# Kernel optimization log

Measured on AMD Instinct MI355X. Metric: run time of the kernel, lower is better.

## Reference

```python
import jax, jax.numpy as jnp
import numpy as np

B, T, C, NH = 8, 1024, 768, 12
HD = C // NH


def setup_inputs() -> dict:
    key = jax.random.key(0)
    k1, k2, k3, k4, k5 = jax.random.split(key, 5)
    s = 0.02
    return {
        "x": jax.random.normal(k1, (B, T, C), dtype=jnp.float32),
        "w_attn": jax.random.normal(k2, (C, 3 * C), dtype=jnp.float32) * s,
        "b_attn": jax.random.normal(k3, (3 * C,), dtype=jnp.float32) * s,
        "w_proj": jax.random.normal(k4, (C, C), dtype=jnp.float32) * s,
        "b_proj": jax.random.normal(k5, (C,), dtype=jnp.float32) * s,
    }


def reference(x, w_attn, b_attn, w_proj, b_proj):
    Bv, Tv, Cv = x.shape
    # fused QKV projection
    qkv = jnp.einsum('btc,cd->btd', x, w_attn) + b_attn  # [B,T,3C]
    q, k, v = jnp.split(qkv, 3, axis=-1)
    # [B, NH, T, HD]
    q = q.reshape(Bv, Tv, NH, HD).transpose(0, 2, 1, 3)
    k = k.reshape(Bv, Tv, NH, HD).transpose(0, 2, 1, 3)
    v = v.reshape(Bv, Tv, NH, HD).transpose(0, 2, 1, 3)
    scale = 1.0 / np.sqrt(HD).astype(np.float32)
    att = jnp.einsum('bhqd,bhkd->bhqk', q, k) * scale  # [B,NH,T,T]
    causal = jnp.tril(jnp.ones((Tv, Tv), dtype=bool))
    att = jnp.where(causal, att, -jnp.inf)
    att = jax.nn.softmax(att, axis=-1)
    y = jnp.einsum('bhqk,bhkd->bhqd', att, v)  # [B,NH,T,HD]
    y = y.transpose(0, 2, 1, 3).reshape(Bv, Tv, Cv)
    return jnp.einsum('btc,cd->btd', y, w_proj) + b_proj
```

## Files before the change

kernel.cpp:

```cpp
#include <hip/hip_runtime.h>

constexpr int kB  = 8;
constexpr int kT  = 1024;
constexpr int kC  = 768;
constexpr int kNH = 12;
constexpr int kHD = 64;
constexpr int kM  = kB * kT;
constexpr int k3C = 3 * kC;
constexpr int kQK = 2 * kC;

using bf16x8 = __attribute__((ext_vector_type(8))) __bf16;
using f32x4  = __attribute__((ext_vector_type(4))) float;

__device__ __forceinline__ unsigned short f2bf(float f) {
    union { float f; unsigned int u; } v; v.f = f;
    unsigned int r = v.u + 0x7fffu + ((v.u >> 16) & 1u);
    return (unsigned short)(r >> 16);
}

__device__ __forceinline__ void async16(const void* g, void* l) {
    __builtin_amdgcn_global_load_lds(
        (__attribute__((address_space(1))) void*)g,
        (__attribute__((address_space(3))) void*)l, 16, 0, 0);
}

template<int IMM> __device__ __forceinline__ void wait_vm() {
    __builtin_amdgcn_s_waitcnt(IMM);
}
__device__ __forceinline__ void wait_vm0() { __builtin_amdgcn_s_waitcnt(0x0F70); }


__global__ __launch_bounds__(256) void cvt_bf16_kernel(
    const float* __restrict__ in, unsigned short* __restrict__ out)
{
    const int i = blockIdx.x * 256 + threadIdx.x;
    const float4 v = ((const float4*)in)[i];
    ushort4 o;
    o.x = f2bf(v.x); o.y = f2bf(v.y); o.z = f2bf(v.z); o.w = f2bf(v.w);
    ((ushort4*)out)[i] = o;
}

__global__ __launch_bounds__(256) void transpose_cvt_kernel(
    const float* __restrict__ W, unsigned short* __restrict__ Wt, int K, int N)
{
    __shared__ float tile[32][33];
    const int tx = threadIdx.x & 31, ty = threadIdx.x >> 5;
    const int n0 = blockIdx.x * 32, k0 = blockIdx.y * 32;
    #pragma unroll
    for (int i = 0; i < 4; ++i)
        tile[ty + i * 8][tx] = W[(size_t)(k0 + ty + i * 8) * N + n0 + tx];
    __syncthreads();
    #pragma unroll
    for (int i = 0; i < 4; ++i)
        Wt[(size_t)(n0 + ty + i * 8) * K + k0 + tx] = f2bf(tile[tx][ty + i * 8]);
}

template<int NSUB, int MODE>
__global__ __launch_bounds__(256) void gemm_mfma_kernel(
    const unsigned short* __restrict__ A, int lda,
    const unsigned short* __restrict__ Bt,
    const float* __restrict__ bias,
    void* __restrict__ outv,
    unsigned short* __restrict__ vt,
    int N, int K)
{
    constexpr int NW = NSUB / 2;
    constexpr int BB = (NSUB / 4 > 0) ? NSUB / 4 : 1;
    constexpr int P  = 2 + BB;
    constexpr int WAIT_P = 0x0F70 | P;

    alignas(16) __shared__ unsigned short As[3][8 * 512];
    alignas(16) __shared__ unsigned short Bs[3][NSUB * 512];

    const int tid  = threadIdx.x;
    const int w    = tid >> 6;
    const int lane = tid & 63;
    const int wr = w >> 1, wc = w & 1;
    const int m0 = blockIdx.y * 128, n0 = blockIdx.x * (NSUB * 16);

    const int fr = lane & 15;
    const int fk = (lane >> 4) * 8;

    auto stage = [&](int bufi, int kt) {
        #pragma unroll
        for (int t = 0; t < 2; ++t) {
            const int fa = w * 2 + t;
            const unsigned short* ga =
                A + (size_t)(m0 + fa * 16 + fr) * lda + kt + fk;
            async16(ga, &As[bufi][fa * 512]);
        }
        #pragma unroll
        for (int t = 0; t < BB; ++t) {
            const int fb = w * BB + t;
            const unsigned short* gb =
                Bt + (size_t)(n0 + fb * 16 + fr) * K + kt + fk;
            async16(gb, &Bs[bufi][fb * 512]);
        }
    };

    f32x4 acc[4][NW];
    #pragma unroll
    for (int i = 0; i < 4; ++i)
        #pragma unroll
        for (int j = 0; j < NW; ++j) {
            f32x4 z = {0.f, 0.f, 0.f, 0.f};
            acc[i][j] = z;
        }

    const int niter = K / 32;
    stage(0, 0);
    stage(1, 32);
    int cur = 0, pf = 2;
    for (int it = 0; it < niter; ++it) {
        if (it + 1 < niter) wait_vm<WAIT_P>();
        else               wait_vm<0x0F70>();
        __builtin_amdgcn_s_barrier();
        if (it + 2 < niter) stage(pf, (it + 2) * 32);

        bf16x8 a[4], b[NW];
        #pragma unroll
        for (int i = 0; i < 4; ++i)
            a[i] = *(const bf16x8*)&As[cur][(wr * 4 + i) * 512 + lane * 8];
        #pragma unroll
        for (int j = 0; j < NW; ++j)
            b[j] = *(const bf16x8*)&Bs[cur][(wc * NW + j) * 512 + lane * 8];
        #pragma unroll
        for (int i = 0; i < 4; ++i)
            #pragma unroll
            for (int j = 0; j < NW; ++j)
                acc[i][j] = __builtin_amdgcn_mfma_f32_16x16x32_bf16(
                    a[i], b[j], acc[i][j], 0, 0, 0);

        cur = (cur == 2) ? 0 : cur + 1;
        pf  = (pf  == 2) ? 0 : pf  + 1;
    }

    const int quad  = lane >> 4;
    const int col16 = lane & 15;
    float biasv[NW];
    #pragma unroll
    for (int j = 0; j < NW; ++j)
        biasv[j] = bias[n0 + wc * (NW * 16) + j * 16 + col16];

    if (MODE == 1 && n0 >= kQK) {
        const int bidx = m0 >> 10;
        #pragma unroll
        for (int i = 0; i < 4; ++i) {
            const int row = m0 + wr * 64 + i * 16 + quad * 4;
            const int t = row & 1023;
            #pragma unroll
            for (int j = 0; j < NW; ++j) {
                const int hv = n0 + wc * (NW * 16) + j * 16 + col16 - kQK;
                const int h = hv >> 6, d = hv & 63;
                ushort4 o;
                o.x = f2bf(acc[i][j][0] + biasv[j]);
                o.y = f2bf(acc[i][j][1] + biasv[j]);
                o.z = f2bf(acc[i][j][2] + biasv[j]);
                o.w = f2bf(acc[i][j][3] + biasv[j]);
                *(ushort4*)&vt[((size_t)(bidx * kNH + h) * kHD + d) * kT + t] = o;
            }
        }
    } else {
        #pragma unroll
        for (int i = 0; i < 4; ++i) {
            #pragma unroll
            for (int r = 0; r < 4; ++r) {
                const int row = m0 + wr * 64 + i * 16 + quad * 4 + r;
                #pragma unroll
                for (int j = 0; j < NW; ++j) {
                    const int col = n0 + wc * (NW * 16) + j * 16 + col16;
                    const float v = acc[i][j][r] + biasv[j];
                    if (MODE == 1)
                        ((unsigned short*)outv)[(size_t)row * kQK + col] = f2bf(v);
                    else
                        ((float*)outv)[(size_t)row * N + col] = v;
                }
            }
        }
    }
}

__global__ __launch_bounds__(256) void attn_mfma_kernel(
    const unsigned short* __restrict__ qkv2,
    const unsigned short* __restrict__ VT,
    unsigned short* __restrict__ y)
{
    alignas(16) __shared__ unsigned short Kf[2][8 * 512];
    alignas(16) __shared__ unsigned short Vf[2][8 * 512];
    alignas(16) __shared__ unsigned short Pf[8 * 512];

    const int tid  = threadIdx.x;
    const int w    = tid >> 6;
    const int lane = tid & 63;
    const int quad = lane >> 4, l15 = lane & 15;
    const int bh  = blockIdx.x >> 3;
    const int b   = bh / kNH, h = bh % kNH;
    const int pid = blockIdx.x & 7;

    auto stage = [&](int bufi, int kbase) {
        const unsigned short* gk = qkv2 +
            (size_t)(b * kT + kbase + w * 16 + l15) * kQK + kC + h * kHD + quad * 8;
        async16(gk,      &Kf[bufi][(w * 2 + 0) * 512]);
        async16(gk + 32, &Kf[bufi][(w * 2 + 1) * 512]);
        const unsigned short* gv = VT +
            ((size_t)bh * kHD + w * 16 + l15) * kT + kbase + quad * 8;
        async16(gv,      &Vf[bufi][(w * 2 + 0) * 512]);
        async16(gv + 32, &Vf[bufi][(w * 2 + 1) * 512]);
    };

    #pragma unroll 1
    for (int phase = 0; phase < 2; ++phase) {
        const int t0 = (phase == 0 ? (15 - pid) : pid) * 64;
        const int nchunks = t0 / 64 + 1;

        __syncthreads();
        stage(0, 0);
        {
            const unsigned short* g0 = qkv2 +
                (size_t)(b * kT + t0 + w * 16 + l15) * kQK + h * kHD + quad * 8;
            async16(g0,      &Pf[(w * 2 + 0) * 512]);
            async16(g0 + 32, &Pf[(w * 2 + 1) * 512]);
        }
        wait_vm0();
        const bf16x8 aq0 = *(const bf16x8*)&Pf[(w * 2 + 0) * 512 + lane * 8];
        const bf16x8 aq1 = *(const bf16x8*)&Pf[(w * 2 + 1) * 512 + lane * 8];

        float m_run[4], l_run[4];
        f32x4 acc_o[4];
        #pragma unroll
        for (int r = 0; r < 4; ++r) { m_run[r] = -INFINITY; l_run[r] = 0.f; }
        #pragma unroll
        for (int n = 0; n < 4; ++n) {
            f32x4 z = {0.f, 0.f, 0.f, 0.f};
            acc_o[n] = z;
        }

        for (int c = 0; c < nchunks; ++c) {
            const int kbase = c * 64;
            const int buf = c & 1;
            wait_vm0();
            __syncthreads();
            if (c + 1 < nchunks) stage(1 - buf, kbase + 64);

            f32x4 acc_s[4];
            #pragma unroll
            for (int k = 0; k < 4; ++k) {
                f32x4 z = {0.f, 0.f, 0.f, 0.f};
                acc_s[k] = z;
            }
            #pragma unroll
            for (int ksub = 0; ksub < 4; ++ksub) {
                const bf16x8 bk0 =
                    *(const bf16x8*)&Kf[buf][(ksub * 2 + 0) * 512 + lane * 8];
                const bf16x8 bk1 =
                    *(const bf16x8*)&Kf[buf][(ksub * 2 + 1) * 512 + lane * 8];
                acc_s[ksub] = __builtin_amdgcn_mfma_f32_16x16x32_bf16(
                    aq0, bk0, acc_s[ksub], 0, 0, 0);
                acc_s[ksub] = __builtin_amdgcn_mfma_f32_16x16x32_bf16(
                    aq1, bk1, acc_s[ksub], 0, 0, 0);
            }

            float sv[4][4];
            #pragma unroll
            for (int ksub = 0; ksub < 4; ++ksub)
                #pragma unroll
                for (int r = 0; r < 4; ++r)
                    sv[ksub][r] = acc_s[ksub][r] * 0.125f;
            if (kbase == t0) {
                const int qrow = t0 + w * 16 + quad * 4;
                #pragma unroll
                for (int ksub = 0; ksub < 4; ++ksub) {
                    const int key = kbase + ksub * 16 + l15;
                    #pragma unroll
                    for (int r = 0; r < 4; ++r)
                        if (key > qrow + r) sv[ksub][r] = -INFINITY;
                }
            }

            float alpha[4];
            #pragma unroll
            for (int r = 0; r < 4; ++r) {
                float mx = fmaxf(fmaxf(sv[0][r], sv[1][r]),
                                 fmaxf(sv[2][r], sv[3][r]));
                mx = fmaxf(mx, __shfl_xor(mx, 1));
                mx = fmaxf(mx, __shfl_xor(mx, 2));
                mx = fmaxf(mx, __shfl_xor(mx, 4));
                mx = fmaxf(mx, __shfl_xor(mx, 8));
                const float m_new = fmaxf(m_run[r], mx);
                alpha[r] = __expf(m_run[r] - m_new);
                float ps = 0.f;
                #pragma unroll
                for (int ksub = 0; ksub < 4; ++ksub) {
                    sv[ksub][r] = __expf(sv[ksub][r] - m_new);
                    ps += sv[ksub][r];
                }
                ps += __shfl_xor(ps, 1);
                ps += __shfl_xor(ps, 2);
                ps += __shfl_xor(ps, 4);
                ps += __shfl_xor(ps, 8);
                l_run[r] = l_run[r] * alpha[r] + ps;
                m_run[r] = m_new;
            }

            #pragma unroll
            for (int ksub = 0; ksub < 4; ++ksub) {
                const int key = ksub * 16 + l15;
                #pragma unroll
                for (int r = 0; r < 4; ++r) {
                    const int lp = quad * 4 + r + ((key & 31) >> 3) * 16;
                    Pf[(w * 2 + (key >> 5)) * 512 + lp * 8 + (key & 7)] =
                        f2bf(sv[ksub][r]);
                }
            }

            #pragma unroll
            for (int n = 0; n < 4; ++n)
                #pragma unroll
                for (int r = 0; r < 4; ++r)
                    acc_o[n][r] *= alpha[r];
            const bf16x8 ap0 = *(const bf16x8*)&Pf[(w * 2 + 0) * 512 + lane * 8];
            const bf16x8 ap1 = *(const bf16x8*)&Pf[(w * 2 + 1) * 512 + lane * 8];
            #pragma unroll
            for (int nsub = 0; nsub < 4; ++nsub) {
                const bf16x8 bv0 =
                    *(const bf16x8*)&Vf[buf][(nsub * 2 + 0) * 512 + lane * 8];
                const bf16x8 bv1 =
                    *(const bf16x8*)&Vf[buf][(nsub * 2 + 1) * 512 + lane * 8];
                acc_o[nsub] = __builtin_amdgcn_mfma_f32_16x16x32_bf16(
                    ap0, bv0, acc_o[nsub], 0, 0, 0);
                acc_o[nsub] = __builtin_amdgcn_mfma_f32_16x16x32_bf16(
                    ap1, bv1, acc_o[nsub], 0, 0, 0);
            }
        }

        float inv[4];
        #pragma unroll
        for (int r = 0; r < 4; ++r) inv[r] = 1.0f / l_run[r];
        #pragma unroll
        for (int nsub = 0; nsub < 4; ++nsub)
            #pragma unroll
            for (int r = 0; r < 4; ++r)
                y[(size_t)(b * kT + t0 + w * 16 + quad * 4 + r) * kC +
                  h * kHD + nsub * 16 + l15] = f2bf(acc_o[nsub][r] * inv[r]);
    }
}

extern "C" void kernel_launch(void* const* d_in, const int* in_sizes, int n_in,
                              void* d_out, int out_size, void* d_ws, size_t ws_size,
                              hipStream_t stream) {
    const float* x      = (const float*)d_in[0];
    const float* w_attn = (const float*)d_in[1];
    const float* b_attn = (const float*)d_in[2];
    const float* w_proj = (const float*)d_in[3];
    const float* b_proj = (const float*)d_in[4];
    float* out = (float*)d_out;

    unsigned short* xb     = (unsigned short*)d_ws;
    unsigned short* wattnT = xb     + (size_t)kM * kC;
    unsigned short* wprojT = wattnT + (size_t)k3C * kC;
    unsigned short* qkv2   = wprojT + (size_t)kC * kC;
    unsigned short* VT     = qkv2   + (size_t)kM * kQK;
    unsigned short* yb     = VT     + (size_t)kNH * kB * kHD * kT;

    cvt_bf16_kernel<<<(kM * kC) / (4 * 256), 256, 0, stream>>>(x, xb);
    transpose_cvt_kernel<<<dim3(k3C / 32, kC / 32), 256, 0, stream>>>(
        w_attn, wattnT, kC, k3C);
    transpose_cvt_kernel<<<dim3(kC / 32, kC / 32), 256, 0, stream>>>(
        w_proj, wprojT, kC, kC);

    gemm_mfma_kernel<8, 1><<<dim3(k3C / 128, kM / 128), 256, 0, stream>>>(
        xb, kC, wattnT, b_attn, qkv2, VT, k3C, kC);

    attn_mfma_kernel<<<kB * kNH * 8, 256, 0, stream>>>(qkv2, VT, yb);

    gemm_mfma_kernel<4, 0><<<dim3(kC / 64, kM / 128), 256, 0, stream>>>(
        yb, kC, wprojT, b_proj, out, nullptr, kC, kC);
}
```

Baseline: 236.8 us.

## Replace LDS-staged block GEMM with per-wave register-direct 64x64 tiles

The GEMM kernel no longer stages A and B tiles through shared memory with async global-to-LDS loads and barriers. Each wave now owns its own 64x64 output tile, loads MFMA fragments directly from global memory into registers, and double-buffers them across k-steps. This removes LDS traffic and block-level synchronisation. In exchange, waves in a block no longer share operand data, so global and L2 load traffic rises and loads are less coalesced.

```diff
diff --git a/kernel.cpp b/kernel.cpp
--- a/kernel.cpp
+++ b/kernel.cpp
@@ -23,10 +23,6 @@
         (__attribute__((address_space(1))) void*)g,
         (__attribute__((address_space(3))) void*)l, 16, 0, 0);
 }
-
-template<int IMM> __device__ __forceinline__ void wait_vm() {
-    __builtin_amdgcn_s_waitcnt(IMM);
-}
 __device__ __forceinline__ void wait_vm0() { __builtin_amdgcn_s_waitcnt(0x0F70); }
 
 
@@ -55,102 +51,94 @@
         Wt[(size_t)(n0 + ty + i * 8) * K + k0 + tx] = f2bf(tile[tx][ty + i * 8]);
 }
 
-template<int NSUB, int MODE>
+template<int MODE>
 __global__ __launch_bounds__(256) void gemm_mfma_kernel(
-    const unsigned short* __restrict__ A, int lda,
+    const unsigned short* __restrict__ A,
     const unsigned short* __restrict__ Bt,
     const float* __restrict__ bias,
     void* __restrict__ outv,
     unsigned short* __restrict__ vt,
     int N, int K)
 {
-    constexpr int NW = NSUB / 2;
-    constexpr int BB = (NSUB / 4 > 0) ? NSUB / 4 : 1;
-    constexpr int P  = 2 + BB;
-    constexpr int WAIT_P = 0x0F70 | P;
-
-    alignas(16) __shared__ unsigned short As[3][8 * 512];
-    alignas(16) __shared__ unsigned short Bs[3][NSUB * 512];
-
-    const int tid  = threadIdx.x;
-    const int w    = tid >> 6;
-    const int lane = tid & 63;
-    const int wr = w >> 1, wc = w & 1;
-    const int m0 = blockIdx.y * 128, n0 = blockIdx.x * (NSUB * 16);
-
-    const int fr = lane & 15;
-    const int fk = (lane >> 4) * 8;
-
-    auto stage = [&](int bufi, int kt) {
-        #pragma unroll
-        for (int t = 0; t < 2; ++t) {
-            const int fa = w * 2 + t;
-            const unsigned short* ga =
-                A + (size_t)(m0 + fa * 16 + fr) * lda + kt + fk;
-            async16(ga, &As[bufi][fa * 512]);
-        }
-        #pragma unroll
-        for (int t = 0; t < BB; ++t) {
-            const int fb = w * BB + t;
-            const unsigned short* gb =
-                Bt + (size_t)(n0 + fb * 16 + fr) * K + kt + fk;
-            async16(gb, &Bs[bufi][fb * 512]);
-        }
-    };
-
-    f32x4 acc[4][NW];
+    const int lane = threadIdx.x & 63;
+    const int w    = threadIdx.x >> 6;
+    const int nt   = N >> 6;
+    const int id   = blockIdx.x * 4 + w;
+    const int tm   = id / nt, tn = id % nt;
+    const int m0   = tm * 64, n0 = tn * 64;
+    const int fr   = lane & 15;
+    const int fk   = (lane >> 4) * 8;
+
+    const unsigned short* ap[4];
+    const unsigned short* bp[4];
+    #pragma unroll
+    for (int i = 0; i < 4; ++i) {
+        ap[i] = A  + (size_t)(m0 + i * 16 + fr) * K + fk;
+        bp[i] = Bt + (size_t)(n0 + i * 16 + fr) * K + fk;
+    }
+
+    f32x4 acc[4][4];
     #pragma unroll
     for (int i = 0; i < 4; ++i)
         #pragma unroll
-        for (int j = 0; j < NW; ++j) {
+        for (int j = 0; j < 4; ++j) {
             f32x4 z = {0.f, 0.f, 0.f, 0.f};
             acc[i][j] = z;
         }
 
-    const int niter = K / 32;
-    stage(0, 0);
-    stage(1, 32);
-    int cur = 0, pf = 2;
-    for (int it = 0; it < niter; ++it) {
-        if (it + 1 < niter) wait_vm<WAIT_P>();
-        else               wait_vm<0x0F70>();
-        __builtin_amdgcn_s_barrier();
-        if (it + 2 < niter) stage(pf, (it + 2) * 32);
-
-        bf16x8 a[4], b[NW];
+    bf16x8 ac[4], bc[4], an[4], bn[4];
+    #pragma unroll
+    for (int i = 0; i < 4; ++i) {
+        ac[i] = *(const bf16x8*)(ap[i]);
+        bc[i] = *(const bf16x8*)(bp[i]);
+        an[i] = *(const bf16x8*)(ap[i] + 32);
+        bn[i] = *(const bf16x8*)(bp[i] + 32);
+    }
+
+    for (int kt = 0; kt < K; kt += 64) {
         #pragma unroll
         for (int i = 0; i < 4; ++i)
-            a[i] = *(const bf16x8*)&As[cur][(wr * 4 + i) * 512 + lane * 8];
-        #pragma unroll
-        for (int j = 0; j < NW; ++j)
-            b[j] = *(const bf16x8*)&Bs[cur][(wc * NW + j) * 512 + lane * 8];
+            #pragma unroll
+            for (int j = 0; j < 4; ++j)
+                acc[i][j] = __builtin_amdgcn_mfma_f32_16x16x32_bf16(
+                    ac[i], bc[j], acc[i][j], 0, 0, 0);
+        if (kt + 64 < K) {
+            #pragma unroll
+            for (int i = 0; i < 4; ++i) {
+                ac[i] = *(const bf16x8*)(ap[i] + kt + 64);
+                bc[i] = *(const bf16x8*)(bp[i] + kt + 64);
+            }
+        }
         #pragma unroll
         for (int i = 0; i < 4; ++i)
             #pragma unroll
-            for (int j = 0; j < NW; ++j)
+            for (int j = 0; j < 4; ++j)
                 acc[i][j] = __builtin_amdgcn_mfma_f32_16x16x32_bf16(
-                    a[i], b[j], acc[i][j], 0, 0, 0);
-
-        cur = (cur == 2) ? 0 : cur + 1;
-        pf  = (pf  == 2) ? 0 : pf  + 1;
+                    an[i], bn[j], acc[i][j], 0, 0, 0);
+        if (kt + 96 < K) {
+            #pragma unroll
+            for (int i = 0; i < 4; ++i) {
+                an[i] = *(const bf16x8*)(ap[i] + kt + 96);
+                bn[i] = *(const bf16x8*)(bp[i] + kt + 96);
+            }
+        }
     }
 
     const int quad  = lane >> 4;
     const int col16 = lane & 15;
-    float biasv[NW];
-    #pragma unroll
-    for (int j = 0; j < NW; ++j)
-        biasv[j] = bias[n0 + wc * (NW * 16) + j * 16 + col16];
+    float biasv[4];
+    #pragma unroll
+    for (int j = 0; j < 4; ++j)
+        biasv[j] = bias[n0 + j * 16 + col16];
 
     if (MODE == 1 && n0 >= kQK) {
         const int bidx = m0 >> 10;
         #pragma unroll
         for (int i = 0; i < 4; ++i) {
-            const int row = m0 + wr * 64 + i * 16 + quad * 4;
-            const int t = row & 1023;
-            #pragma unroll
-            for (int j = 0; j < NW; ++j) {
-                const int hv = n0 + wc * (NW * 16) + j * 16 + col16 - kQK;
+            const int t = (m0 + i * 16 + quad * 4) & 1023;
+            #pragma unroll
+            for (int j = 0; j < 4; ++j) {
+                const int hv = n0 + j * 16 + col16 - kQK;
                 const int h = hv >> 6, d = hv & 63;
                 ushort4 o;
                 o.x = f2bf(acc[i][j][0] + biasv[j]);
@@ -165,10 +153,10 @@
         for (int i = 0; i < 4; ++i) {
             #pragma unroll
             for (int r = 0; r < 4; ++r) {
-                const int row = m0 + wr * 64 + i * 16 + quad * 4 + r;
-                #pragma unroll
-                for (int j = 0; j < NW; ++j) {
-                    const int col = n0 + wc * (NW * 16) + j * 16 + col16;
+                const int row = m0 + i * 16 + quad * 4 + r;
+                #pragma unroll
+                for (int j = 0; j < 4; ++j) {
+                    const int col = n0 + j * 16 + col16;
                     const float v = acc[i][j][r] + biasv[j];
                     if (MODE == 1)
                         ((unsigned short*)outv)[(size_t)row * kQK + col] = f2bf(v);
@@ -368,11 +356,11 @@
     transpose_cvt_kernel<<<dim3(kC / 32, kC / 32), 256, 0, stream>>>(
         w_proj, wprojT, kC, kC);
 
-    gemm_mfma_kernel<8, 1><<<dim3(k3C / 128, kM / 128), 256, 0, stream>>>(
-        xb, kC, wattnT, b_attn, qkv2, VT, k3C, kC);
+    gemm_mfma_kernel<1><<<(kM / 64) * (k3C / 64) / 4, 256, 0, stream>>>(
+        xb, wattnT, b_attn, qkv2, VT, k3C, kC);
 
     attn_mfma_kernel<<<kB * kNH * 8, 256, 0, stream>>>(qkv2, VT, yb);
 
-    gemm_mfma_kernel<4, 0><<<dim3(kC / 64, kM / 128), 256, 0, stream>>>(
-        yb, kC, wprojT, b_proj, out, nullptr, kC, kC);
-}
+    gemm_mfma_kernel<0><<<(kM / 64) * (kC / 64) / 4, 256, 0, stream>>>(
+        yb, wprojT, b_proj, out, nullptr, kC, kC);
+}
```

After: 299.3 us. 26.4% more time.
